# Optimization experiments

Measured on AMD Instinct MI355X. Metric: run time of the kernel, lower is better.

Reference implementation:

```python
import jax, jax.numpy as jnp
import numpy as np

HID = 32


def setup_inputs() -> dict:
    key = jax.random.key(0)
    ks = jax.random.split(key, 16)
    T = 4096
    s_grid = jnp.arange(T, dtype=jnp.float32)  # monotone time grid, h = 1
    y0 = jax.random.normal(ks[0], (4,), dtype=jnp.float32)
    sc = 0.3  # modest init scale
    Win = jax.random.normal(ks[1], (HID, 5), dtype=jnp.float32) * sc
    bin_ = jax.random.normal(ks[2], (HID,), dtype=jnp.float32) * 0.05
    W1a = jax.random.normal(ks[3], (HID, HID), dtype=jnp.float32) * sc / np.sqrt(HID)
    b1a = jax.random.normal(ks[4], (HID,), dtype=jnp.float32) * 0.05
    W1b = jax.random.normal(ks[5], (HID, HID), dtype=jnp.float32) * sc / np.sqrt(HID)
    b1b = jax.random.normal(ks[6], (HID,), dtype=jnp.float32) * 0.05
    W2a = jax.random.normal(ks[7], (HID, HID), dtype=jnp.float32) * sc / np.sqrt(HID)
    b2a = jax.random.normal(ks[8], (HID,), dtype=jnp.float32) * 0.05
    W2b = jax.random.normal(ks[9], (HID, HID), dtype=jnp.float32) * sc / np.sqrt(HID)
    b2b = jax.random.normal(ks[10], (HID,), dtype=jnp.float32) * 0.05
    Wout = jax.random.normal(ks[11], (4, HID), dtype=jnp.float32) * sc / np.sqrt(HID)
    bout = jax.random.normal(ks[12], (4,), dtype=jnp.float32) * 0.05
    A = jax.random.normal(ks[13], (4,), dtype=jnp.float32) * 0.1
    return {"s_grid": s_grid, "y0": y0, "Win": Win, "bin_": bin_,
            "W1a": W1a, "b1a": b1a, "W1b": W1b, "b1b": b1b,
            "W2a": W2a, "b2a": b2a, "W2b": W2b, "b2b": b2b,
            "Wout": Wout, "bout": bout, "A": A}


def reference(s_grid, y0, Win, bin_, W1a, b1a, W1b, b1b, W2a, b2a, W2b, b2b, Wout, bout, A):
    # Dropout layers are identity in eval mode.
    def f(y, s):
        z = jnp.concatenate([y, s[None]])             # (5,)
        x = jnp.tanh(Win @ z + bin_)                  # (HID,)
        x = x + (W1b @ jnp.tanh(W1a @ x + b1a) + b1b)  # residual block 1
        x = x + (W2b @ jnp.tanh(W2a @ x + b2a) + b2b)  # residual block 2
        net = jax.nn.sigmoid(Wout @ x + bout)          # (4,)
        sy = jax.nn.sigmoid(y)
        return 0.01 * sy * (A - sy) * net

    def step(y, sh):
        s_prev, h = sh
        # NOTE: original code evaluates all k's at s_grid[i-1]
        k1 = f(y, s_prev)
        k2 = f(y + 0.5 * h * k1, s_prev)
        k3 = f(y + 0.5 * h * k2, s_prev)
        k4 = f(y + h * k3, s_prev)
        y_next = y + h / 6.0 * (k1 + 2.0 * k2 + 2.0 * k3 + k4)
        return y_next, y_next

    s_prev = s_grid[:-1]
    h = s_grid[1:] - s_grid[:-1]
    _, ys = jax.lax.scan(step, y0, (s_prev, h))
    return jnp.concatenate([y0[None, :], ys], axis=0)  # (T, 4)
```

## Files before the change

kernel.cpp:

```cpp
#include <hip/hip_runtime.h>


__device__ __forceinline__ float fexp2(float x) { return __builtin_amdgcn_exp2f(x); }
__device__ __forceinline__ float frcp(float x) { return __builtin_amdgcn_rcpf(x); }
#define C_TANH 2.8853900817779268f
#define C_NSIG (-1.4426950408889634f)

template<int CTRL>
__device__ __forceinline__ float dppmov(float x) {
  return __int_as_float(__builtin_amdgcn_update_dpp(
      0, __float_as_int(x), CTRL, 0xF, 0xF, true));
}
#define RORc(K) (0x120 | (K))

__device__ __forceinline__ void p16swap(float& a, float& b) {
  asm("s_nop 1\n\tv_permlane16_swap_b32 %0, %1" : "+v"(a), "+v"(b));
}
__device__ __forceinline__ void p32swap(float& a, float& b) {
  asm("s_nop 1\n\tv_permlane32_swap_b32 %0, %1" : "+v"(a), "+v"(b));
}

#define MV8(W, BZ, X, SOUT) do {                                       \
    float b0_ = fmaf((X),             W[0], (BZ));                     \
    float b1_ = dppmov<RORc(1)>(X)  * W[1];                            \
    float b2_ = dppmov<RORc(2)>(X)  * W[2];                            \
    float b3_ = dppmov<RORc(3)>(X)  * W[3];                            \
    float b4_ = dppmov<RORc(4)>(X)  * W[4];                            \
    float b5_ = dppmov<RORc(5)>(X)  * W[5];                            \
    float b6_ = dppmov<RORc(6)>(X)  * W[6];                            \
    float b7_ = dppmov<RORc(7)>(X)  * W[7];                            \
    b0_ = fmaf(dppmov<RORc(8)>(X),  W[8],  b0_);                       \
    b1_ = fmaf(dppmov<RORc(9)>(X),  W[9],  b1_);                       \
    b2_ = fmaf(dppmov<RORc(10)>(X), W[10], b2_);                       \
    b3_ = fmaf(dppmov<RORc(11)>(X), W[11], b3_);                       \
    b4_ = fmaf(dppmov<RORc(12)>(X), W[12], b4_);                       \
    b5_ = fmaf(dppmov<RORc(13)>(X), W[13], b5_);                       \
    b6_ = fmaf(dppmov<RORc(14)>(X), W[14], b6_);                       \
    b7_ = fmaf(dppmov<RORc(15)>(X), W[15], b7_);                       \
    SOUT = ((b0_ + b1_) + (b2_ + b3_)) + ((b4_ + b5_) + (b6_ + b7_));  \
  } while (0)

__global__ __launch_bounds__(512, 1) __attribute__((amdgpu_waves_per_eu(2, 2)))
void ode_kernel(const float* __restrict__ s_grid,
                const float* __restrict__ y0in,
                const float* __restrict__ Win,
                const float* __restrict__ bin_,
                const float* __restrict__ W1a, const float* __restrict__ b1a,
                const float* __restrict__ W1b, const float* __restrict__ b1b,
                const float* __restrict__ W2a, const float* __restrict__ b2a,
                const float* __restrict__ W2b, const float* __restrict__ b2b,
                const float* __restrict__ Wout, const float* __restrict__ bout,
                const float* __restrict__ Aarr,
                float* __restrict__ out, int T) {
  const int tid = threadIdx.x;
  const int wv = tid >> 6;
  const int grp = wv >> 2;
  const int st = wv & 3;
  const int lane = tid & 63;
  const int i = lane & 15;
  const int m = lane >> 4;
  const int mlo = m & 1;
  const int mhi = m >> 1;

  __shared__ float s_lds[4096];
  __shared__ float SC[2][8][8];
  for (int idx = tid; idx < T && idx < 4096; idx += 512)
    s_lds[idx] = s_grid[idx];
  __syncthreads();

  int delta;
  {
    float pr = (float)i;
    float pr1 = dppmov<RORc(1)>(pr);
    delta = (((int)pr1) - i) & 15;
  }
  bool p32_c_low;
  {
    float v = (float)(lane >> 5);
    float c = v, d = v;
    p32swap(c, d);
    p32_c_low = (c == 0.0f);
  }

  const int rA = 16 * mhi + i, hA = mlo;
  const int rB = 16 * mlo + i, hB = mhi;
  const int r_in = 16 * mlo + i;
  const int e1 = r_in;

  float w1a[16], w2a[16], m21[16];
#pragma unroll 1
  for (int k = 0; k < 16; ++k) {
    int cA = hA * 16 + ((i + delta * k) & 15);
    int cB = hB * 16 + ((i + delta * k) & 15);
    w1a[k] = W1a[rA * 32 + cA] * (-2.0f * C_TANH);
    w2a[k] = W2a[rA * 32 + cA] * (-2.0f * C_TANH);
    float acc = 0.0f;
    for (int q = 0; q < 32; ++q)
      acc = fmaf(W2a[rB * 32 + q], W1b[q * 32 + cB], acc);
    m21[k] = acc * (-2.0f * C_TANH);
  }
  float bz1a;
  {
    float rs = 0.0f;
    for (int c = 0; c < 32; ++c) rs += W1a[rA * 32 + c];
    bz1a = hA ? 0.0f : C_TANH * (b1a[rA] + rs);
  }
  float c2sel;
  {
    float rs2a = 0.0f, m21rs = 0.0f, wb = 0.0f;
    for (int q = 0; q < 32; ++q) {
      float w2q = W2a[rB * 32 + q];
      rs2a += w2q;
      float rs1bq = 0.0f;
      for (int c = 0; c < 32; ++c) rs1bq += W1b[q * 32 + c];
      m21rs = fmaf(w2q, rs1bq, m21rs);
      wb = fmaf(w2q, b1b[q], wb);
    }
    c2sel = hB ? 0.0f : C_TANH * (rs2a + m21rs + wb + b2a[rB]);
  }
  const bool seedsel = (mlo == mhi);

  float winy0 = Win[r_in * 5 + 0] * C_TANH;
  float winy1 = Win[r_in * 5 + 1] * C_TANH;
  float winy2 = Win[r_in * 5 + 2] * C_TANH;
  float winy3 = Win[r_in * 5 + 3] * C_TANH;
  float wins  = Win[r_in * 5 + 4] * C_TANH;
  float binr  = bin_[r_in] * C_TANH;
  float gsel_a = mhi ? winy2 : winy0;
  float gsel_b = mhi ? winy3 : winy1;

  const int ra_ = 2 * mhi, rb_ = 2 * mhi + 1;
  float woXa = Wout[ra_ * 32 + e1] * (-2.0f * C_NSIG);
  float woXb = Wout[rb_ * 32 + e1] * (-2.0f * C_NSIG);
  float wo1a, wo1b, wo2a, wo2b, boa, bob;
  {
    float w1s_a = 0.0f, w1s_b = 0.0f, w2s_a = 0.0f, w2s_b = 0.0f;
    float rsX_a = 0.0f, rsX_b = 0.0f, rs1_a = 0.0f, rs1_b = 0.0f;
    float rs2_a = 0.0f, rs2_b = 0.0f, bt_a = 0.0f, bt_b = 0.0f;
    for (int q = 0; q < 32; ++q) {
      float waq = Wout[ra_ * 32 + q], wbq = Wout[rb_ * 32 + q];
      w1s_a = fmaf(waq, W1b[q * 32 + e1], w1s_a);
      w1s_b = fmaf(wbq, W1b[q * 32 + e1], w1s_b);
      w2s_a = fmaf(waq, W2b[q * 32 + e1], w2s_a);
      w2s_b = fmaf(wbq, W2b[q * 32 + e1], w2s_b);
      rsX_a += waq; rsX_b += wbq;
      float rs1bq = 0.0f, rs2bq = 0.0f;
      for (int c = 0; c < 32; ++c) {
        rs1bq += W1b[q * 32 + c];
        rs2bq += W2b[q * 32 + c];
      }
      rs1_a = fmaf(waq, rs1bq, rs1_a); rs1_b = fmaf(wbq, rs1bq, rs1_b);
      rs2_a = fmaf(waq, rs2bq, rs2_a); rs2_b = fmaf(wbq, rs2bq, rs2_b);
      float bs = b1b[q] + b2b[q];
      bt_a = fmaf(waq, bs, bt_a); bt_b = fmaf(wbq, bs, bt_b);
    }
    wo1a = w1s_a * (-2.0f * C_NSIG); wo1b = w1s_b * (-2.0f * C_NSIG);
    wo2a = w2s_a * (-2.0f * C_NSIG); wo2b = w2s_b * (-2.0f * C_NSIG);
    boa = (bout[ra_] + bt_a + rsX_a + rs1_a + rs2_a) * (C_NSIG / 32.0f);
    bob = (bout[rb_] + bt_b + rsX_b + rs1_b + rs2_b) * (C_NSIG / 32.0f);
  }
  float Aa = mhi ? Aarr[2] : Aarr[0];
  float Ab = mhi ? Aarr[3] : Aarr[1];

  auto relayout = [&](float v) -> float {
    float c = v, d = v;
    p32swap(c, d);
    float lo = p32_c_low ? c : d;
    float hi = p32_c_low ? d : c;
    return mlo ? hi : lo;
  };

  float pfa, pfb, wpa, wpb, na, nb, gkv;

  auto setpref = [&](float yA, float yB) {
    float sa = frcp(1.0f + fexp2(yA * C_NSIG));
    float sb = frcp(1.0f + fexp2(yB * C_NSIG));
    pfa = 0.01f * sa * (Aa - sa);
    pfb = 0.01f * sb * (Ab - sb);
    wpa = gsel_a * pfa;
    wpb = gsel_b * pfb;
  };

  auto STAGE = [&](float zin) {
    float g0v = frcp(fexp2(zin) + 1.0f);
    float u1; MV8(w1a, bz1a, g0v, u1);
    { float b = u1; p16swap(u1, b); u1 += b; }
    float q2; MV8(w2a, 0.0f, g0v, q2);
    { float b = q2; p16swap(q2, b); q2 += b; }
    float g1 = frcp(fexp2(u1) + 1.0f);
    float g1r = relayout(g1);
    float seed = (seedsel ? q2 : 0.0f) + c2sel;
    float u2; MV8(m21, seed, g1, u2);
    { float b = u2; p32swap(u2, b); u2 += b; }
    float g2 = frcp(fexp2(u2) + 1.0f);
    float ph0 = fmaf(wo1a, g1r, fmaf(woXa, g0v, boa));
    float ph1 = fmaf(wo1b, g1r, fmaf(woXb, g0v, bob));
    float p0 = fmaf(wo2a, g2, ph0);
    float p1 = fmaf(wo2b, g2, ph1);
    p0 += dppmov<RORc(8)>(p0); p1 += dppmov<RORc(8)>(p1);
    p0 += dppmov<RORc(4)>(p0); p1 += dppmov<RORc(4)>(p1);
    p0 += dppmov<RORc(2)>(p0); p1 += dppmov<RORc(2)>(p1);
    p0 += dppmov<RORc(1)>(p0); p1 += dppmov<RORc(1)>(p1);
    { float q = p0; p16swap(p0, q); p0 += q; }
    { float q = p1; p16swap(p1, q); p1 += q; }
    na = frcp(1.0f + fexp2(p0));
    nb = frcp(1.0f + fexp2(p1));
    float gp = fmaf(wpb, nb, wpa * na);
    float gq = gp;
    p32swap(gp, gq);
    gkv = gp + gq;
  };

  auto rdslot = [&](int pp, int ss, float& gk, float& ka, float& kb) {
    float2 kk = *reinterpret_cast<float2*>(&SC[pp][ss][mhi << 1]);
    ka = kk.x; kb = kk.y;
    gk = SC[pp][ss][4];
  };
  auto rd4 = [&](int pp, int base, float& ag, float& aa, float& ab) {
    float g, a, b;
    rdslot(pp, base + 0, g, a, b); ag = g; aa = a; ab = b;
    rdslot(pp, base + 1, g, a, b);
    ag = fmaf(2.0f, g, ag); aa = fmaf(2.0f, a, aa); ab = fmaf(2.0f, b, ab);
    rdslot(pp, base + 2, g, a, b);
    ag = fmaf(2.0f, g, ag); aa = fmaf(2.0f, a, aa); ab = fmaf(2.0f, b, ab);
    rdslot(pp, base + 3, g, a, b); ag += g; aa += a; ab += b;
  };
  auto wrslot = [&](int qq, float Ka, float Kb) {
    float c0 = Ka, d0 = Ka; p32swap(c0, d0);
    float hiKa = p32_c_low ? d0 : c0;
    float c1 = Kb, d1 = Kb; p32swap(c1, d1);
    float hiKb = p32_c_low ? d1 : c1;
    if (lane == 0) {
      *reinterpret_cast<float4*>(&SC[qq][wv][0]) =
          make_float4(Ka, Kb, hiKa, hiKb);
      SC[qq][wv][4] = gkv;
    }
  };

  float y00 = y0in[0], y01 = y0in[1], y02 = y0in[2], y03 = y0in[3];
  float ya = mhi ? y02 : y00;
  float yb = mhi ? y03 : y01;

  if (wv == 0 && (lane & 0x1E) == 0)
    out[(lane >> 4) + (lane & 1)] = (lane & 1) ? yb : ya;

  float zb = fmaf(winy0, y00, fmaf(winy1, y01, fmaf(winy2, y02,
             fmaf(winy3, y03, fmaf(wins, s_lds[0], binr)))));

  {
    float s0v = s_lds[0];
    float s1v = (T > 1) ? s_lds[1] : s0v;
    float h0 = s1v - s0v;
    setpref(ya, yb);
    STAGE(grp ? fmaf(wins, h0, zb) : zb);
    wrslot(1, pfa * na, pfb * nb);
  }
  __syncthreads();

  float h6p0 = 0.0f, h6p1 = 0.0f, hsumP = 0.0f;
  const int NJ = T >> 1;

  for (int j = 0; j < NJ; ++j) {
    const int w = j & 1, r = w ^ 1;
    int i0 = 2 * j, i1 = 2 * j + 1, i2v = 2 * j + 2;
    float s0v = s_lds[i0];
    float s1v = s_lds[i1 < T ? i1 : T - 1];
    float s2v = s_lds[i2v < T ? i2v : T - 1];
    float h0 = s1v - s0v, h1 = s2v - s1v;
    float h6_0 = h0 * (1.0f / 6.0f), h6_1 = h1 * (1.0f / 6.0f);

    float gC0, aC0, bC0, gC1, aC1, bC1;
    rd4(r, 0, gC0, aC0, bC0);
    rd4(r, 4, gC1, aC1, bC1);
    const int sl = st ? st - 1 : 0;
    float g0i, a0i, b0i, g1i, a1i, b1i;
    rdslot(r, sl, g0i, a0i, b0i);
    rdslot(r, 4 + sl, g1i, a1i, b1i);

    if (j) {
      float yam = fmaf(h6p0, aC0, ya);
      float ybm = fmaf(h6p0, bC0, yb);
      ya = fmaf(h6p1, aC1, yam);
      yb = fmaf(h6p1, bC1, ybm);
      zb = fmaf(h6p1, gC1, fmaf(h6p0, gC0, fmaf(wins, hsumP, zb)));
      if (wv == 0 && (lane & 0x1E) == 0) {
        const size_t t0 = (size_t)(2 * j - 1);
        const int c = (lane >> 4) + (lane & 1);
        out[t0 * 4 + c] = (lane & 1) ? ybm : yam;
        out[(t0 + 1) * 4 + c] = (lane & 1) ? yb : ya;
      }
    }

    float gin, kain, kbin;
    if (grp == 0) {
      gin = 2.0f * g1i - g0i;
      kain = 2.0f * a1i - a0i;
      kbin = 2.0f * b1i - b0i;
    } else {
      gin = 3.0f * g1i - 2.0f * g0i;
      kain = 3.0f * a1i - 2.0f * a0i;
      kbin = 3.0f * b1i - 2.0f * b0i;
    }

    float yA, yB, zB, hg;
    if (grp == 0) {
      yA = ya; yB = yb; zB = zb; hg = h0;
    } else {
      float cga = 2.0f * aC1 - aC0;
      float cgb = 2.0f * bC1 - bC0;
      float cgg = 2.0f * gC1 - gC0;
      yA = fmaf(h6_0, cga, ya);
      yB = fmaf(h6_0, cgb, yb);
      zB = fmaf(h6_0, cgg, fmaf(wins, h0, zb));
      hg = h1;
    }
    float cw = (st == 0) ? 0.0f : (st == 3) ? hg : 0.5f * hg;

    setpref(fmaf(cw, kain, yA), fmaf(cw, kbin, yB));
    STAGE(fmaf(cw, gin, zB));
    wrslot(w, pfa * na, pfb * nb);

    h6p0 = h6_0; h6p1 = h6_1; hsumP = h0 + h1;
    __syncthreads();
  }

  if (T > 1) {
    const int r = (NJ - 1) & 1;
    float gE, aE, bE;
    rd4(r, 0, gE, aE, bE);
    (void)gE;
    float yaf = fmaf(h6p0, aE, ya);
    float ybf = fmaf(h6p0, bE, yb);
    if (wv == 0 && (lane & 0x1E) == 0)
      out[(size_t)(T - 1) * 4 + (lane >> 4) + (lane & 1)] =
          (lane & 1) ? ybf : yaf;
  }
}

extern "C" void kernel_launch(void* const* d_in, const int* in_sizes, int n_in,
                              void* d_out, int out_size, void* d_ws, size_t ws_size,
                              hipStream_t stream) {
  const float* s_grid = (const float*)d_in[0];
  const float* y0 = (const float*)d_in[1];
  const float* Win = (const float*)d_in[2];
  const float* bin_ = (const float*)d_in[3];
  const float* W1a = (const float*)d_in[4];
  const float* b1a = (const float*)d_in[5];
  const float* W1b = (const float*)d_in[6];
  const float* b1b = (const float*)d_in[7];
  const float* W2a = (const float*)d_in[8];
  const float* b2a = (const float*)d_in[9];
  const float* W2b = (const float*)d_in[10];
  const float* b2b = (const float*)d_in[11];
  const float* Wout = (const float*)d_in[12];
  const float* bout = (const float*)d_in[13];
  const float* A = (const float*)d_in[14];
  int T = in_sizes[0];

  ode_kernel<<<1, 512, 0, stream>>>(s_grid, y0, Win, bin_, W1a, b1a, W1b, b1b,
                                    W2a, b2a, W2b, b2b, Wout, bout, A,
                                    (float*)d_out, T);
}
```

Measured before the change: 2.324 ms.

## Fuse DPP rotations into mul/fmac and restructure LDS stage-result exchange

The matrix-vector macro now uses inline-asm v_mul_f32_dpp and v_fmac_f32_dpp, so each row rotation feeds the arithmetic directly instead of going through a separate DPP move. The shared exchange buffer is split into a packed float2 array per half-wave and a separate gk array. Writers store directly from lanes 0 and 32, which removes the permlane32 swaps. Readers fetch the RK stage values with a few float4 LDS loads instead of many scalar ones. Together these shorten the serial per-step critical path, at the cost of hand-written asm that depends on correct DPP hazard handling.

```diff
diff --git a/kernel.cpp b/kernel.cpp
--- a/kernel.cpp
+++ b/kernel.cpp
@@ -20,24 +20,32 @@
   asm("s_nop 1\n\tv_permlane32_swap_b32 %0, %1" : "+v"(a), "+v"(b));
 }
 
-#define MV8(W, BZ, X, SOUT) do {                                       \
-    float b0_ = fmaf((X),             W[0], (BZ));                     \
-    float b1_ = dppmov<RORc(1)>(X)  * W[1];                            \
-    float b2_ = dppmov<RORc(2)>(X)  * W[2];                            \
-    float b3_ = dppmov<RORc(3)>(X)  * W[3];                            \
-    float b4_ = dppmov<RORc(4)>(X)  * W[4];                            \
-    float b5_ = dppmov<RORc(5)>(X)  * W[5];                            \
-    float b6_ = dppmov<RORc(6)>(X)  * W[6];                            \
-    float b7_ = dppmov<RORc(7)>(X)  * W[7];                            \
-    b0_ = fmaf(dppmov<RORc(8)>(X),  W[8],  b0_);                       \
-    b1_ = fmaf(dppmov<RORc(9)>(X),  W[9],  b1_);                       \
-    b2_ = fmaf(dppmov<RORc(10)>(X), W[10], b2_);                       \
-    b3_ = fmaf(dppmov<RORc(11)>(X), W[11], b3_);                       \
-    b4_ = fmaf(dppmov<RORc(12)>(X), W[12], b4_);                       \
-    b5_ = fmaf(dppmov<RORc(13)>(X), W[13], b5_);                       \
-    b6_ = fmaf(dppmov<RORc(14)>(X), W[14], b6_);                       \
-    b7_ = fmaf(dppmov<RORc(15)>(X), W[15], b7_);                       \
-    SOUT = ((b0_ + b1_) + (b2_ + b3_)) + ((b4_ + b5_) + (b6_ + b7_));  \
+#define MV8(W, BZ, X, SOUT) do {                                            \
+    float b0_ = fmaf((X), W[0], (BZ));                                      \
+    float b1_, b2_, b3_, b4_, b5_, b6_, b7_;                                \
+    asm("s_nop 1\n\t"                                                       \
+        "v_mul_f32_dpp %1, %8, %9 row_ror:1 row_mask:0xf bank_mask:0xf\n\t" \
+        "v_mul_f32_dpp %2, %8, %10 row_ror:2 row_mask:0xf bank_mask:0xf\n\t"\
+        "v_mul_f32_dpp %3, %8, %11 row_ror:3 row_mask:0xf bank_mask:0xf\n\t"\
+        "v_mul_f32_dpp %4, %8, %12 row_ror:4 row_mask:0xf bank_mask:0xf\n\t"\
+        "v_mul_f32_dpp %5, %8, %13 row_ror:5 row_mask:0xf bank_mask:0xf\n\t"\
+        "v_mul_f32_dpp %6, %8, %14 row_ror:6 row_mask:0xf bank_mask:0xf\n\t"\
+        "v_mul_f32_dpp %7, %8, %15 row_ror:7 row_mask:0xf bank_mask:0xf\n\t"\
+        "v_fmac_f32_dpp %0, %8, %16 row_ror:8 row_mask:0xf bank_mask:0xf\n\t"\
+        "v_fmac_f32_dpp %1, %8, %17 row_ror:9 row_mask:0xf bank_mask:0xf\n\t"\
+        "v_fmac_f32_dpp %2, %8, %18 row_ror:10 row_mask:0xf bank_mask:0xf\n\t"\
+        "v_fmac_f32_dpp %3, %8, %19 row_ror:11 row_mask:0xf bank_mask:0xf\n\t"\
+        "v_fmac_f32_dpp %4, %8, %20 row_ror:12 row_mask:0xf bank_mask:0xf\n\t"\
+        "v_fmac_f32_dpp %5, %8, %21 row_ror:13 row_mask:0xf bank_mask:0xf\n\t"\
+        "v_fmac_f32_dpp %6, %8, %22 row_ror:14 row_mask:0xf bank_mask:0xf\n\t"\
+        "v_fmac_f32_dpp %7, %8, %23 row_ror:15 row_mask:0xf bank_mask:0xf"  \
+        : "+v"(b0_), "=&v"(b1_), "=&v"(b2_), "=&v"(b3_),                    \
+          "=&v"(b4_), "=&v"(b5_), "=&v"(b6_), "=&v"(b7_)                    \
+        : "v"(X), "v"(W[1]), "v"(W[2]), "v"(W[3]), "v"(W[4]),               \
+          "v"(W[5]), "v"(W[6]), "v"(W[7]), "v"(W[8]), "v"(W[9]),            \
+          "v"(W[10]), "v"(W[11]), "v"(W[12]), "v"(W[13]), "v"(W[14]),       \
+          "v"(W[15]));                                                      \
+    SOUT = ((b0_ + b1_) + (b2_ + b3_)) + ((b4_ + b5_) + (b6_ + b7_));       \
   } while (0)
 
 __global__ __launch_bounds__(512, 1) __attribute__((amdgpu_waves_per_eu(2, 2)))
@@ -63,7 +71,8 @@
   const int mhi = m >> 1;
 
   __shared__ float s_lds[4096];
-  __shared__ float SC[2][8][8];
+  __shared__ __align__(16) float2 PK[2][2][8];
+  __shared__ __align__(16) float GK[2][8];
   for (int idx = tid; idx < T && idx < 4096; idx += 512)
     s_lds[idx] = s_grid[idx];
   __syncthreads();
@@ -211,30 +220,11 @@
     gkv = gp + gq;
   };
 
-  auto rdslot = [&](int pp, int ss, float& gk, float& ka, float& kb) {
-    float2 kk = *reinterpret_cast<float2*>(&SC[pp][ss][mhi << 1]);
-    ka = kk.x; kb = kk.y;
-    gk = SC[pp][ss][4];
-  };
-  auto rd4 = [&](int pp, int base, float& ag, float& aa, float& ab) {
-    float g, a, b;
-    rdslot(pp, base + 0, g, a, b); ag = g; aa = a; ab = b;
-    rdslot(pp, base + 1, g, a, b);
-    ag = fmaf(2.0f, g, ag); aa = fmaf(2.0f, a, aa); ab = fmaf(2.0f, b, ab);
-    rdslot(pp, base + 2, g, a, b);
-    ag = fmaf(2.0f, g, ag); aa = fmaf(2.0f, a, aa); ab = fmaf(2.0f, b, ab);
-    rdslot(pp, base + 3, g, a, b); ag += g; aa += a; ab += b;
-  };
   auto wrslot = [&](int qq, float Ka, float Kb) {
-    float c0 = Ka, d0 = Ka; p32swap(c0, d0);
-    float hiKa = p32_c_low ? d0 : c0;
-    float c1 = Kb, d1 = Kb; p32swap(c1, d1);
-    float hiKb = p32_c_low ? d1 : c1;
-    if (lane == 0) {
-      *reinterpret_cast<float4*>(&SC[qq][wv][0]) =
-          make_float4(Ka, Kb, hiKa, hiKb);
-      SC[qq][wv][4] = gkv;
-    }
+    if ((lane & 31) == 0)
+      PK[qq][mhi][wv] = make_float2(Ka, Kb);
+    if (lane == 0)
+      GK[qq][wv] = gkv;
   };
 
   float y00 = y0in[0], y01 = y0in[1], y02 = y0in[2], y03 = y0in[3];
@@ -269,13 +259,23 @@
     float h0 = s1v - s0v, h1 = s2v - s1v;
     float h6_0 = h0 * (1.0f / 6.0f), h6_1 = h1 * (1.0f / 6.0f);
 
-    float gC0, aC0, bC0, gC1, aC1, bC1;
-    rd4(r, 0, gC0, aC0, bC0);
-    rd4(r, 4, gC1, aC1, bC1);
+    float4 pva = *(const float4*)&PK[r][mhi][0];
+    float4 pvb = *(const float4*)&PK[r][mhi][2];
+    float4 pvc = *(const float4*)&PK[r][mhi][4];
+    float4 pvd = *(const float4*)&PK[r][mhi][6];
+    float4 gva = *(const float4*)&GK[r][0];
+    float4 gvb = *(const float4*)&GK[r][4];
+    float aC0 = fmaf(2.0f, pva.z, pva.x); aC0 = fmaf(2.0f, pvb.x, aC0); aC0 += pvb.z;
+    float bC0 = fmaf(2.0f, pva.w, pva.y); bC0 = fmaf(2.0f, pvb.y, bC0); bC0 += pvb.w;
+    float gC0 = fmaf(2.0f, gva.y, gva.x); gC0 = fmaf(2.0f, gva.z, gC0); gC0 += gva.w;
+    float aC1 = fmaf(2.0f, pvc.z, pvc.x); aC1 = fmaf(2.0f, pvd.x, aC1); aC1 += pvd.z;
+    float bC1 = fmaf(2.0f, pvc.w, pvc.y); bC1 = fmaf(2.0f, pvd.y, bC1); bC1 += pvd.w;
+    float gC1 = fmaf(2.0f, gvb.y, gvb.x); gC1 = fmaf(2.0f, gvb.z, gC1); gC1 += gvb.w;
     const int sl = st ? st - 1 : 0;
-    float g0i, a0i, b0i, g1i, a1i, b1i;
-    rdslot(r, sl, g0i, a0i, b0i);
-    rdslot(r, 4 + sl, g1i, a1i, b1i);
+    float2 pk0 = PK[r][mhi][sl];
+    float2 pk1 = PK[r][mhi][4 + sl];
+    float g0i = GK[r][sl], g1i = GK[r][4 + sl];
+    float a0i = pk0.x, b0i = pk0.y, a1i = pk1.x, b1i = pk1.y;
 
     if (j) {
       float yam = fmaf(h6p0, aC0, ya);
@@ -325,10 +325,11 @@
   }
 
   if (T > 1) {
-    const int r = (NJ - 1) & 1;
-    float gE, aE, bE;
-    rd4(r, 0, gE, aE, bE);
-    (void)gE;
+    const int rr = (NJ - 1) & 1;
+    float4 pva = *(const float4*)&PK[rr][mhi][0];
+    float4 pvb = *(const float4*)&PK[rr][mhi][2];
+    float aE = fmaf(2.0f, pva.z, pva.x); aE = fmaf(2.0f, pvb.x, aE); aE += pvb.z;
+    float bE = fmaf(2.0f, pva.w, pva.y); bE = fmaf(2.0f, pvb.y, bE); bE += pvb.w;
     float yaf = fmaf(h6p0, aE, ya);
     float ybf = fmaf(h6p0, bE, yb);
     if (wv == 0 && (lane & 0x1E) == 0)
```

New measurement: 1.964 ms. -15.5%, faster.
